# Performance work log

Measured on AMD Instinct MI355X. Metric: run time of the kernel, lower is better.

The kernel has to match this reference:

```python
import jax, jax.numpy as jnp
import numpy as np

N = 20000
E = 320000
F_IN = 256
HID = 32
HEADS = 8
EDGE_DIM = HID // 4  # 8
NEG_SLOPE = 0.2


def _gat_conv(x, src, dst, e_emb, W, att_s, att_d, W_e, att_e, bias, H, C):
    """PyG-style GATConv with edge_dim, add_self_loops=True (fill_value='mean'), concat heads."""
    n = x.shape[0]
    loop = jnp.arange(n, dtype=src.dtype)
    # self-loop edge_attr = scatter-mean of edge_attr by dst (0 for isolated nodes)
    deg = jax.ops.segment_sum(jnp.ones_like(dst, dtype=x.dtype), dst, num_segments=n)
    e_mean = jax.ops.segment_sum(e_emb, dst, num_segments=n) / jnp.maximum(deg, 1.0)[:, None]
    src_a = jnp.concatenate([src, loop])
    dst_a = jnp.concatenate([dst, loop])
    e_all = jnp.concatenate([e_emb, e_mean], axis=0)  # [E+N, edge_dim]

    h = (x @ W).reshape(n, H, C)                      # [N,H,C]
    a_src = jnp.einsum('nhc,hc->nh', h, att_s)        # [N,H]
    a_dst = jnp.einsum('nhc,hc->nh', h, att_d)
    he = (e_all @ W_e).reshape(-1, H, C)              # [E+N,H,C]
    a_edge = jnp.einsum('ehc,hc->eh', he, att_e)      # [E+N,H]

    alpha = jax.nn.leaky_relu(a_src[src_a] + a_dst[dst_a] + a_edge, NEG_SLOPE)
    # segment softmax over destination nodes
    amax = jax.ops.segment_max(alpha, dst_a, num_segments=n)
    alpha = jnp.exp(alpha - amax[dst_a])
    denom = jax.ops.segment_sum(alpha, dst_a, num_segments=n)
    alpha = alpha / (denom[dst_a] + 1e-16)

    msg = h[src_a] * alpha[:, :, None]                # [E+N,H,C]
    out = jax.ops.segment_sum(msg, dst_a, num_segments=n)  # [N,H,C]
    return out.reshape(n, H * C) + bias


def setup_inputs() -> dict:
    key = jax.random.key(0)
    ks = jax.random.split(key, 16)

    def glorot(k, shape):
        fan_in, fan_out = shape[0], shape[-1]
        s = np.sqrt(6.0 / (fan_in + fan_out))
        return jax.random.uniform(k, shape, jnp.float32, -s, s)

    x = jax.random.normal(ks[0], (N, F_IN), jnp.float32)
    edge_index = jax.random.randint(ks[1], (2, E), 0, N, jnp.int32)
    edge_attr = jax.random.uniform(ks[2], (E, 2), jnp.float32)

    # spatial_embed: Linear(2 -> EDGE_DIM)
    Wse = glorot(ks[3], (2, EDGE_DIM))
    bse = jnp.zeros((EDGE_DIM,), jnp.float32)
    # conv1: in=F_IN, heads=HEADS, out=HID, edge_dim=EDGE_DIM
    W1 = glorot(ks[4], (F_IN, HEADS * HID))
    as1 = glorot(ks[5], (HEADS, HID))
    ad1 = glorot(ks[6], (HEADS, HID))
    We1 = glorot(ks[7], (EDGE_DIM, HEADS * HID))
    ae1 = glorot(ks[8], (HEADS, HID))
    b1 = jnp.zeros((HEADS * HID,), jnp.float32)
    # conv2: in=HEADS*HID, heads=1, out=HID
    W2 = glorot(ks[9], (HEADS * HID, HID))
    as2 = glorot(ks[10], (1, HID))
    ad2 = glorot(ks[11], (1, HID))
    We2 = glorot(ks[12], (EDGE_DIM, HID))
    ae2 = glorot(ks[13], (1, HID))
    b2 = jnp.zeros((HID,), jnp.float32)

    return {"x": x, "edge_index": edge_index, "edge_attr": edge_attr,
            "Wse": Wse, "bse": bse,
            "W1": W1, "as1": as1, "ad1": ad1, "We1": We1, "ae1": ae1, "b1": b1,
            "W2": W2, "as2": as2, "ad2": ad2, "We2": We2, "ae2": ae2, "b2": b2}


def reference(x, edge_index, edge_attr, Wse, bse,
              W1, as1, ad1, We1, ae1, b1,
              W2, as2, ad2, We2, ae2, b2):
    src, dst = edge_index[0], edge_index[1]
    e = jax.nn.relu(edge_attr @ Wse + bse)            # [E, EDGE_DIM]
    h = _gat_conv(x, src, dst, e, W1, as1, ad1, We1, ae1, b1, HEADS, HID)
    h = jax.nn.relu(h)                                # dropout inactive (eval)
    out = _gat_conv(h, src, dst, e, W2, as2, ad2, We2, ae2, b2, 1, HID)
    return out
```

## Files before the change

### kernel.cpp

```cpp
#include <hip/hip_runtime.h>
#include <hip/hip_bf16.h>
#include <hip/hip_fp16.h>
#include <float.h>


typedef short v8s __attribute__((ext_vector_type(8)));
typedef float v4f __attribute__((ext_vector_type(4)));

__device__ __forceinline__ ushort f2bf(float f) {
  unsigned u = __float_as_uint(f);
  u = (u + 0x7FFF + ((u >> 16) & 1)) >> 16;
  return (ushort)u;
}
__device__ __forceinline__ float bf2f(ushort h) {
  return __uint_as_float(((unsigned)h) << 16);
}
__device__ __forceinline__ unsigned pk2bf(float lo, float hi) {
  return (unsigned)f2bf(lo) | ((unsigned)f2bf(hi) << 16);
}
__device__ __forceinline__ unsigned pk2h(float lo, float hi) {
  return (unsigned)__half_as_ushort(__float2half(lo)) |
         ((unsigned)__half_as_ushort(__float2half(hi)) << 16);
}

__global__ __launch_bounds__(256) void k_pre(const int* __restrict__ dst,
                                             const float* __restrict__ W1,
                                             const float* __restrict__ We1,
                                             const float* __restrict__ ae1,
                                             const float* __restrict__ We2,
                                             const float* __restrict__ ae2,
                                             const float* __restrict__ W2,
                                             int* __restrict__ deg,
                                             ushort* __restrict__ Bt,
                                             float* __restrict__ M1,
                                             float* __restrict__ m2,
                                             float* __restrict__ W2B,
                                             int E, int DB) {
  int b = blockIdx.x;
  if (b < DB) {
    int e = b * 256 + threadIdx.x;
    if (e < E) atomicAdd(&deg[dst[e]], 1);
    return;
  }
  if (b == DB + 64) {
    int t = threadIdx.x;
    for (int i = t; i < 8192; i += 256) {
      int k = i >> 5, cc = i & 31;
      W2B[(size_t)(k >> 2) * 128 + cc * 4 + (k & 3)] = W2[(size_t)k * 32 + cc];
    }
    if (t < 64) {
      int k = t >> 3, h = t & 7;
      float s = 0.f;
      for (int c = 0; c < 32; c++) s += We1[k * 256 + h * 32 + c] * ae1[h * 32 + c];
      M1[k * 8 + h] = s;
    } else if (t < 72) {
      int k = t - 64;
      float s = 0.f;
      for (int c = 0; c < 32; c++) s += We2[k * 32 + c] * ae2[c];
      m2[k] = s;
    }
    return;
  }
  int b2 = b - DB;
  __shared__ float tile[32][33];
  int bx = b2 & 7, by = b2 >> 3;
  int tx = threadIdx.x & 31, ty = threadIdx.x >> 5;
  for (int r = ty; r < 32; r += 8)
    tile[r][tx] = W1[(size_t)(by * 32 + r) * 256 + bx * 32 + tx];
  __syncthreads();
  for (int r = ty; r < 32; r += 8)
    Bt[(size_t)(bx * 32 + r) * 256 + by * 32 + tx] = f2bf(tile[tx][r]);
}

__global__ __launch_bounds__(1024) void k_scan(const int* __restrict__ deg,
                                               int* __restrict__ row_ptr,
                                               int* __restrict__ cursor, int N) {
  __shared__ int part[1024];
  int tid = threadIdx.x;
  int chunk = (N + 1023) / 1024;
  int lo = tid * chunk;
  if (lo > N) lo = N;
  int hi = lo + chunk;
  if (hi > N) hi = N;
  int s = 0;
  for (int i = lo; i < hi; i++) { s += deg[i]; cursor[i] = 0; }
  part[tid] = s;
  __syncthreads();
  for (int off = 1; off < 1024; off <<= 1) {
    int v = 0;
    if (tid >= off) v = part[tid - off];
    __syncthreads();
    part[tid] += v;
    __syncthreads();
  }
  int base = part[tid] - s;
  for (int i = lo; i < hi; i++) { row_ptr[i] = base; base += deg[i]; }
  if (tid == 1023) row_ptr[N] = part[1023];
}

__global__ __launch_bounds__(256) void k_mega1(
    const float* __restrict__ A, const ushort* __restrict__ Bt,
    const float* __restrict__ as1, const float* __restrict__ ad1,
    ushort* __restrict__ h1b, float* __restrict__ asv, float* __restrict__ adv, int M,
    const int* __restrict__ src, const int* __restrict__ dst,
    const float* __restrict__ ea, const float* __restrict__ Wse,
    const float* __restrict__ bse, const float* __restrict__ M1,
    const float* __restrict__ m2, const int* __restrict__ row_ptr,
    int* __restrict__ cursor, char* __restrict__ rec, int E, int GB) {
  __shared__ __align__(16) char smem[27648];
  int t = threadIdx.x;
  if (blockIdx.x >= GB) {
    float* sW  = (float*)smem;
    float* sbv = sW + 16;
    float* sM  = sbv + 8;
    float* sm2 = sM + 64;
    if (t < 16) sW[t] = Wse[t];
    if (t < 8) sbv[t] = bse[t];
    if (t < 64) sM[t] = M1[t];
    if (t >= 64 && t < 72) sm2[t - 64] = m2[t - 64];
    __syncthreads();
    int i = (blockIdx.x - GB) * 256 + t;
    if (i >= E) return;
    float2 av = ((const float2*)ea)[i];
    float e8[8];
#pragma unroll
    for (int k = 0; k < 8; k++)
      e8[k] = fmaxf(av.x * sW[k] + av.y * sW[8 + k] + sbv[k], 0.f);
    float o[8];
#pragma unroll
    for (int h = 0; h < 8; h++) {
      float s = 0.f;
#pragma unroll
      for (int k = 0; k < 8; k++) s += e8[k] * sM[k * 8 + h];
      o[h] = s;
    }
    float s2 = 0.f;
#pragma unroll
    for (int k = 0; k < 8; k++) s2 += e8[k] * sm2[k];
    int d = dst[i];
    int pos = row_ptr[d] + atomicAdd(&cursor[d], 1);
    uint4 w0, w1;
    w0.x = (unsigned)src[i];
    w0.y = pk2h(o[0], o[1]);
    w0.z = pk2h(o[2], o[3]);
    w0.w = pk2h(o[4], o[5]);
    w1.x = pk2h(o[6], o[7]);
    w1.y = __float_as_uint(s2);
    w1.z = 0; w1.w = 0;
    *(uint4*)(rec + (size_t)pos * 32)      = w0;
    *(uint4*)(rec + (size_t)pos * 32 + 16) = w1;
    return;
  }
  ushort* sA = (ushort*)smem;
  ushort* sB = (ushort*)(smem + 5120);
  float* sas = (float*)(smem + 25600);
  float* sad = (float*)(smem + 26624);
  int wave = t >> 6, lane = t & 63;
  int m0 = blockIdx.x * 64;
  int c = lane & 15, kg = lane >> 4;
  sas[t] = as1[t];
  sad[t] = ad1[t];
  v4f acc[4][4];
#pragma unroll
  for (int a = 0; a < 4; a++)
#pragma unroll
    for (int b = 0; b < 4; b++) acc[a][b] = (v4f)(0.f);
  int arow = t >> 2;
  int akoff = (t & 3) * 8;
  bool aval = (m0 + arow) < M;
  const float* aptr = A + (size_t)(m0 + arow) * 256 + akoff;
  const ushort* bptr = Bt + (size_t)t * 256;
  for (int k0 = 0; k0 < 256; k0 += 32) {
    float4 v0 = make_float4(0.f, 0.f, 0.f, 0.f), v1 = v0;
    if (aval) { v0 = *(const float4*)(aptr + k0); v1 = *(const float4*)(aptr + k0 + 4); }
    unsigned* dst32 = (unsigned*)&sA[arow * 40 + akoff];
    dst32[0] = pk2bf(v0.x, v0.y);
    dst32[1] = pk2bf(v0.z, v0.w);
    dst32[2] = pk2bf(v1.x, v1.y);
    dst32[3] = pk2bf(v1.z, v1.w);
    *(v8s*)&sB[t * 40 + 0]  = *(const v8s*)(bptr + k0 + 0);
    *(v8s*)&sB[t * 40 + 8]  = *(const v8s*)(bptr + k0 + 8);
    *(v8s*)&sB[t * 40 + 16] = *(const v8s*)(bptr + k0 + 16);
    *(v8s*)&sB[t * 40 + 24] = *(const v8s*)(bptr + k0 + 24);
    __syncthreads();
    v8s af[4], bfr[4];
#pragma unroll
    for (int mt = 0; mt < 4; mt++) af[mt] = *(v8s*)&sA[(mt * 16 + c) * 40 + kg * 8];
#pragma unroll
    for (int nt = 0; nt < 4; nt++) bfr[nt] = *(v8s*)&sB[(wave * 64 + nt * 16 + c) * 40 + kg * 8];
#pragma unroll
    for (int mt = 0; mt < 4; mt++)
#pragma unroll
      for (int nt = 0; nt < 4; nt++)
        acc[mt][nt] = __builtin_amdgcn_mfma_f32_16x16x32_bf16(af[mt], bfr[nt], acc[mt][nt], 0, 0, 0);
    __syncthreads();
  }
  int colbase = wave * 64;
#pragma unroll
  for (int mt = 0; mt < 4; mt++) {
#pragma unroll
    for (int i = 0; i < 4; i++) {
      int m = m0 + mt * 16 + kg * 4 + i;
      if (m < M) {
#pragma unroll
        for (int nt = 0; nt < 4; nt++)
          h1b[(size_t)m * 256 + colbase + nt * 16 + c] = f2bf(acc[mt][nt][i]);
      }
      float s1a = acc[mt][0][i] * sas[colbase + c]      + acc[mt][1][i] * sas[colbase + 16 + c];
      float s2a = acc[mt][0][i] * sad[colbase + c]      + acc[mt][1][i] * sad[colbase + 16 + c];
      float s1b = acc[mt][2][i] * sas[colbase + 32 + c] + acc[mt][3][i] * sas[colbase + 48 + c];
      float s2b = acc[mt][2][i] * sad[colbase + 32 + c] + acc[mt][3][i] * sad[colbase + 48 + c];
#pragma unroll
      for (int o = 1; o < 16; o <<= 1) {
        s1a += __shfl_xor(s1a, o);
        s2a += __shfl_xor(s2a, o);
        s1b += __shfl_xor(s1b, o);
        s2b += __shfl_xor(s2b, o);
      }
      if (c == 0 && m < M) {
        asv[(size_t)m * 8 + 2 * wave]     = s1a;
        adv[(size_t)m * 8 + 2 * wave]     = s2a;
        asv[(size_t)m * 8 + 2 * wave + 1] = s1b;
        adv[(size_t)m * 8 + 2 * wave + 1] = s2b;
      }
    }
  }
}

__global__ __launch_bounds__(64) void k_conv1(
    const int* __restrict__ row_ptr, const char* __restrict__ rec,
    const float* __restrict__ asv, const float* __restrict__ adv,
    const ushort* __restrict__ h1b, const float* __restrict__ b1,
    const float* __restrict__ W2B, const float* __restrict__ as2,
    const float* __restrict__ ad2, float* __restrict__ g2,
    float* __restrict__ asv2, float* __restrict__ adv2, int N) {
  int n = blockIdx.x;
  int lane = threadIdx.x;
  int h = lane >> 3;
  int sub = lane & 7;
  int hh = lane & 7;
  __shared__ float sw[64 * 8];
  __shared__ int ssrc[64];
  __shared__ float sm[8], sl[8], sadv[8], smean[8];
  __shared__ float sh2[256];
  int begin = row_ptr[n], end = row_ptr[n + 1];
  int degr = end - begin;
  if (lane < 8) { sm[lane] = -FLT_MAX; sl[lane] = 0.f; sadv[lane] = adv[(size_t)n * 8 + lane]; }
  float aedsum = 0.f;
  float4 acc = make_float4(0.f, 0.f, 0.f, 0.f);
  for (int cs = begin; cs < end; cs += 64) {
    int c = min(64, end - cs);
    __syncthreads();
    if (lane < c) ssrc[lane] = *(const int*)(rec + (size_t)(cs + lane) * 32);
    __syncthreads();
    for (int idx = lane; idx < c * 8; idx += 64) {
      int el = idx >> 3;
      float ae = __half2float(*(const __half*)(rec + (size_t)(cs + el) * 32 + 4 + hh * 2));
      aedsum += ae;
      float a = asv[(size_t)ssrc[el] * 8 + hh] + sadv[hh] + ae;
      a = a > 0.f ? a : 0.2f * a;
      sw[idx] = a;
    }
    __syncthreads();
    float mloc = -FLT_MAX;
    for (int el = sub; el < c; el += 8) mloc = fmaxf(mloc, sw[el * 8 + h]);
#pragma unroll
    for (int o = 1; o < 8; o <<= 1) mloc = fmaxf(mloc, __shfl_xor(mloc, o));
    float mold = sm[h];
    float mnew = fmaxf(mold, mloc);
    float scale = __expf(mold - mnew);
    float lloc = 0.f;
    for (int el = sub; el < c; el += 8) {
      float w = __expf(sw[el * 8 + h] - mnew);
      sw[el * 8 + h] = w;
      lloc += w;
    }
#pragma unroll
    for (int o = 1; o < 8; o <<= 1) lloc += __shfl_xor(lloc, o);
    __syncthreads();
    if (sub == 0) { sm[h] = mnew; sl[h] = sl[h] * scale + lloc; }
    acc.x *= scale; acc.y *= scale; acc.z *= scale; acc.w *= scale;
#pragma unroll 2
    for (int el = 0; el < c; el++) {
      float w = sw[el * 8 + h];
      ushort4 hv = *(const ushort4*)(h1b + (size_t)ssrc[el] * 256 + lane * 4);
      acc.x += w * bf2f(hv.x);
      acc.y += w * bf2f(hv.y);
      acc.z += w * bf2f(hv.z);
      acc.w += w * bf2f(hv.w);
    }
  }
  aedsum += __shfl_xor(aedsum, 8);
  aedsum += __shfl_xor(aedsum, 16);
  aedsum += __shfl_xor(aedsum, 32);
  float invd = 1.f / (float)(degr > 1 ? degr : 1);
  if (lane < 8) smean[lane] = aedsum * invd;
  __syncthreads();
  float a_self = asv[(size_t)n * 8 + h] + sadv[h] + smean[h];
  a_self = a_self > 0.f ? a_self : 0.2f * a_self;
  float mold = sm[h];
  float mnew = fmaxf(mold, a_self);
  float scale = __expf(mold - mnew);
  float w_self = __expf(a_self - mnew);
  float l_fin = sl[h] * scale + w_self;
  ushort4 hs = *(const ushort4*)(h1b + (size_t)n * 256 + lane * 4);
  acc.x = acc.x * scale + w_self * bf2f(hs.x);
  acc.y = acc.y * scale + w_self * bf2f(hs.y);
  acc.z = acc.z * scale + w_self * bf2f(hs.z);
  acc.w = acc.w * scale + w_self * bf2f(hs.w);
  float inv = 1.f / (l_fin + 1e-16f);
  float4 bv = *(const float4*)(b1 + lane * 4);
  float4 h2v;
  h2v.x = fmaxf(acc.x * inv + bv.x, 0.f);
  h2v.y = fmaxf(acc.y * inv + bv.y, 0.f);
  h2v.z = fmaxf(acc.z * inv + bv.z, 0.f);
  h2v.w = fmaxf(acc.w * inv + bv.w, 0.f);
  *(float4*)&sh2[lane * 4] = h2v;
  __syncthreads();
  int half = lane >> 5, cc = lane & 31;
  const float* wp = W2B + (size_t)half * 32 * 128 + cc * 4;
  const float* hp2 = sh2 + half * 128;
  float part = 0.f;
#pragma unroll 8
  for (int g = 0; g < 32; g++) {
    float4 wv = *(const float4*)(wp + g * 128);
    float4 hv = *(const float4*)(hp2 + g * 4);
    part += wv.x * hv.x + wv.y * hv.y + wv.z * hv.z + wv.w * hv.w;
  }
  part += __shfl_xor(part, 32);
  float s1 = part * as2[cc];
  float s2 = part * ad2[cc];
#pragma unroll
  for (int o = 1; o < 32; o <<= 1) {
    s1 += __shfl_xor(s1, o);
    s2 += __shfl_xor(s2, o);
  }
  if (lane < 32) g2[(size_t)n * 32 + cc] = part;
  if (lane == 0) { asv2[n] = s1; adv2[n] = s2; }
}

__global__ __launch_bounds__(64) void k_conv2(
    const int* __restrict__ row_ptr, const char* __restrict__ rec,
    const float* __restrict__ asv2, const float* __restrict__ adv2,
    const float* __restrict__ g2, const float* __restrict__ b2,
    float* __restrict__ out, int N) {
  int n = blockIdx.x;
  int lane = threadIdx.x;
  int sub = lane >> 3, q = lane & 7;
  __shared__ float sw[64];
  __shared__ int ssrc[64];
  int begin = row_ptr[n], end = row_ptr[n + 1];
  int degr = end - begin;
  float advn = adv2[n];
  float m = -FLT_MAX, l = 0.f, aedsum = 0.f;
  float4 acc = make_float4(0.f, 0.f, 0.f, 0.f);
  for (int cs = begin; cs < end; cs += 64) {
    int c = min(64, end - cs);
    __syncthreads();
    float a = -FLT_MAX;
    if (lane < c) {
      const char* rp = rec + (size_t)(cs + lane) * 32;
      int s = *(const int*)rp;
      ssrc[lane] = s;
      float ae = *(const float*)(rp + 20);
      aedsum += ae;
      a = asv2[s] + advn + ae;
      a = a > 0.f ? a : 0.2f * a;
    }
    float cm = a;
#pragma unroll
    for (int o = 1; o < 64; o <<= 1) cm = fmaxf(cm, __shfl_xor(cm, o));
    float nm = fmaxf(m, cm);
    float sc = __expf(m - nm);
    float w = (lane < c) ? __expf(a - nm) : 0.f;
    float cl = w;
#pragma unroll
    for (int o = 1; o < 64; o <<= 1) cl += __shfl_xor(cl, o);
    l = l * sc + cl;
    m = nm;
    sw[lane] = w;
    __syncthreads();
    acc.x *= sc; acc.y *= sc; acc.z *= sc; acc.w *= sc;
    for (int el = sub; el < c; el += 8) {
      float w2 = sw[el];
      const float4 gv = *(const float4*)(g2 + (size_t)ssrc[el] * 32 + q * 4);
      acc.x += w2 * gv.x; acc.y += w2 * gv.y; acc.z += w2 * gv.z; acc.w += w2 * gv.w;
    }
  }
#pragma unroll
  for (int o = 1; o < 64; o <<= 1) aedsum += __shfl_xor(aedsum, o);
  float invd = 1.f / (float)(degr > 1 ? degr : 1);
  float a_self = asv2[n] + advn + aedsum * invd;
  a_self = a_self > 0.f ? a_self : 0.2f * a_self;
  float nm = fmaxf(m, a_self);
  float sc = __expf(m - nm);
  float w_self = __expf(a_self - nm);
  l = l * sc + w_self;
  acc.x *= sc; acc.y *= sc; acc.z *= sc; acc.w *= sc;
  if (sub == 0) {
    const float4 gv = *(const float4*)(g2 + (size_t)n * 32 + q * 4);
    acc.x += w_self * gv.x; acc.y += w_self * gv.y;
    acc.z += w_self * gv.z; acc.w += w_self * gv.w;
  }
#pragma unroll
  for (int o = 8; o < 64; o <<= 1) {
    acc.x += __shfl_xor(acc.x, o);
    acc.y += __shfl_xor(acc.y, o);
    acc.z += __shfl_xor(acc.z, o);
    acc.w += __shfl_xor(acc.w, o);
  }
  if (lane < 8) {
    float inv = 1.f / (l + 1e-16f);
    float4 bv = *(const float4*)(b2 + lane * 4);
    float4 o4;
    o4.x = acc.x * inv + bv.x;
    o4.y = acc.y * inv + bv.y;
    o4.z = acc.z * inv + bv.z;
    o4.w = acc.w * inv + bv.w;
    *(float4*)(out + (size_t)n * 32 + lane * 4) = o4;
  }
}

extern "C" void kernel_launch(void* const* d_in, const int* in_sizes, int n_in,
                              void* d_out, int out_size, void* d_ws, size_t ws_size,
                              hipStream_t stream) {
  (void)n_in; (void)out_size; (void)ws_size;
  const float* x   = (const float*)d_in[0];
  const int*   ei  = (const int*)d_in[1];
  const float* ea  = (const float*)d_in[2];
  const float* Wse = (const float*)d_in[3];
  const float* bse = (const float*)d_in[4];
  const float* W1  = (const float*)d_in[5];
  const float* as1 = (const float*)d_in[6];
  const float* ad1 = (const float*)d_in[7];
  const float* We1 = (const float*)d_in[8];
  const float* ae1 = (const float*)d_in[9];
  const float* b1  = (const float*)d_in[10];
  const float* W2  = (const float*)d_in[11];
  const float* as2 = (const float*)d_in[12];
  const float* ad2 = (const float*)d_in[13];
  const float* We2 = (const float*)d_in[14];
  const float* ae2 = (const float*)d_in[15];
  const float* b2  = (const float*)d_in[16];
  const int N = in_sizes[0] / 256;
  const int E = in_sizes[1] / 2;
  const int* src = ei;
  const int* dst = ei + E;

  char* base = (char*)d_ws;
  size_t off = 0;
  auto alloc = [&](size_t bytes) -> char* {
    off = (off + 255) & ~(size_t)255;
    char* p = base + off;
    off += bytes;
    return p;
  };
  int*   deg      = (int*)alloc((size_t)N * 4);
  int*   cursor   = (int*)alloc((size_t)N * 4);
  int* row_ptr    = (int*)alloc((size_t)(N + 1) * 4);
  char* rec       = alloc((size_t)E * 32);
  ushort* W1T     = (ushort*)alloc((size_t)256 * 256 * 2);
  float* W2B      = (float*)alloc((size_t)256 * 32 * 4);
  ushort* h1b     = (ushort*)alloc((size_t)N * 256 * 2);
  float* asv1     = (float*)alloc((size_t)N * 8 * 4);
  float* adv1     = (float*)alloc((size_t)N * 8 * 4);
  float* g2       = (float*)alloc((size_t)N * 32 * 4);
  float* asv2     = (float*)alloc((size_t)N * 4);
  float* adv2     = (float*)alloc((size_t)N * 4);
  float* M1       = (float*)alloc(64 * 4);
  float* m2       = (float*)alloc(8 * 4);

  const int DB = (E + 255) / 256;
  const int GB = (N + 63) / 64;
  hipMemsetAsync(deg, 0, (size_t)N * 4, stream);
  k_pre<<<DB + 65, 256, 0, stream>>>(dst, W1, We1, ae1, We2, ae2, W2,
                                     deg, W1T, M1, m2, W2B, E, DB);
  k_scan<<<1, 1024, 0, stream>>>(deg, row_ptr, cursor, N);
  k_mega1<<<GB + DB, 256, 0, stream>>>(x, W1T, as1, ad1, h1b, asv1, adv1, N,
                                       src, dst, ea, Wse, bse, M1, m2, row_ptr,
                                       cursor, rec, E, GB);
  k_conv1<<<N, 64, 0, stream>>>(row_ptr, rec, asv1, adv1, h1b, b1,
                                W2B, as2, ad2, g2, asv2, adv2, N);
  k_conv2<<<N, 64, 0, stream>>>(row_ptr, rec, asv2, adv2, g2, b2, (float*)d_out, N);
}
```

Baseline: 227.8 us.

## Pack four destination nodes per block in GAT conv kernels and batch gathers

Both aggregation kernels now run four nodes per 256-thread block, one wavefront each, instead of one 64-thread block per node. Chunk loops iterate to the block's maximum chunk count so __syncthreads stays uniform, and invalid or exhausted waves are masked. The conv1 gather loop is unrolled by eight to issue independent h1 row loads together, and conv2's gather gets unroll 2. This is meant to cut launch and scheduling overhead from very small blocks and raise memory-level parallelism. The cost is block-level syncs coupling waves, so a high-degree node stalls the other three waves in its block.

After: 245.0 us. +7.5%, slower.

```diff
diff --git a/kernel.cpp b/kernel.cpp
--- a/kernel.cpp
+++ b/kernel.cpp
@@ -227,63 +227,91 @@
   }
 }
 
-__global__ __launch_bounds__(64) void k_conv1(
+__global__ __launch_bounds__(256) void k_conv1(
     const int* __restrict__ row_ptr, const char* __restrict__ rec,
     const float* __restrict__ asv, const float* __restrict__ adv,
     const ushort* __restrict__ h1b, const float* __restrict__ b1,
     const float* __restrict__ W2B, const float* __restrict__ as2,
     const float* __restrict__ ad2, float* __restrict__ g2,
     float* __restrict__ asv2, float* __restrict__ adv2, int N) {
-  int n = blockIdx.x;
-  int lane = threadIdx.x;
+  int wid = threadIdx.x >> 6;
+  int lane = threadIdx.x & 63;
+  int n = blockIdx.x * 4 + wid;
+  bool valid = n < N;
   int h = lane >> 3;
   int sub = lane & 7;
   int hh = lane & 7;
-  __shared__ float sw[64 * 8];
-  __shared__ int ssrc[64];
-  __shared__ float sm[8], sl[8], sadv[8], smean[8];
-  __shared__ float sh2[256];
-  int begin = row_ptr[n], end = row_ptr[n + 1];
+  __shared__ float sw[4][64 * 8];
+  __shared__ int ssrc[4][64];
+  __shared__ float sm[4][8], sl[4][8], sadv[4][8], smean[4][8];
+  __shared__ float sh2[4][256];
+  __shared__ int snch[4];
+  int begin = 0, end = 0;
+  if (valid) { begin = row_ptr[n]; end = row_ptr[n + 1]; }
   int degr = end - begin;
-  if (lane < 8) { sm[lane] = -FLT_MAX; sl[lane] = 0.f; sadv[lane] = adv[(size_t)n * 8 + lane]; }
+  if (lane == 0) snch[wid] = (degr + 63) >> 6;
+  if (lane < 8) {
+    sm[wid][lane] = -FLT_MAX;
+    sl[wid][lane] = 0.f;
+    sadv[wid][lane] = valid ? adv[(size_t)n * 8 + lane] : 0.f;
+  }
+  __syncthreads();
+  int maxc = max(max(snch[0], snch[1]), max(snch[2], snch[3]));
   float aedsum = 0.f;
   float4 acc = make_float4(0.f, 0.f, 0.f, 0.f);
-  for (int cs = begin; cs < end; cs += 64) {
+  for (int ch = 0; ch < maxc; ch++) {
+    int cs = begin + ch * 64;
     int c = min(64, end - cs);
     __syncthreads();
-    if (lane < c) ssrc[lane] = *(const int*)(rec + (size_t)(cs + lane) * 32);
+    if (lane < c) ssrc[wid][lane] = *(const int*)(rec + (size_t)(cs + lane) * 32);
     __syncthreads();
     for (int idx = lane; idx < c * 8; idx += 64) {
       int el = idx >> 3;
       float ae = __half2float(*(const __half*)(rec + (size_t)(cs + el) * 32 + 4 + hh * 2));
       aedsum += ae;
-      float a = asv[(size_t)ssrc[el] * 8 + hh] + sadv[hh] + ae;
+      float a = asv[(size_t)ssrc[wid][el] * 8 + hh] + sadv[wid][hh] + ae;
       a = a > 0.f ? a : 0.2f * a;
-      sw[idx] = a;
+      sw[wid][idx] = a;
     }
     __syncthreads();
     float mloc = -FLT_MAX;
-    for (int el = sub; el < c; el += 8) mloc = fmaxf(mloc, sw[el * 8 + h]);
+    for (int el = sub; el < c; el += 8) mloc = fmaxf(mloc, sw[wid][el * 8 + h]);
 #pragma unroll
     for (int o = 1; o < 8; o <<= 1) mloc = fmaxf(mloc, __shfl_xor(mloc, o));
-    float mold = sm[h];
+    float mold = sm[wid][h];
     float mnew = fmaxf(mold, mloc);
     float scale = __expf(mold - mnew);
     float lloc = 0.f;
     for (int el = sub; el < c; el += 8) {
-      float w = __expf(sw[el * 8 + h] - mnew);
-      sw[el * 8 + h] = w;
+      float w = __expf(sw[wid][el * 8 + h] - mnew);
+      sw[wid][el * 8 + h] = w;
       lloc += w;
     }
 #pragma unroll
     for (int o = 1; o < 8; o <<= 1) lloc += __shfl_xor(lloc, o);
     __syncthreads();
-    if (sub == 0) { sm[h] = mnew; sl[h] = sl[h] * scale + lloc; }
+    if (sub == 0 && c > 0) { sm[wid][h] = mnew; sl[wid][h] = sl[wid][h] * scale + lloc; }
     acc.x *= scale; acc.y *= scale; acc.z *= scale; acc.w *= scale;
-#pragma unroll 2
-    for (int el = 0; el < c; el++) {
-      float w = sw[el * 8 + h];
-      ushort4 hv = *(const ushort4*)(h1b + (size_t)ssrc[el] * 256 + lane * 4);
+    int el = 0;
+    for (; el + 8 <= c; el += 8) {
+      float w[8];
+      ushort4 hv[8];
+#pragma unroll
+      for (int j = 0; j < 8; j++) w[j] = sw[wid][(el + j) * 8 + h];
+#pragma unroll
+      for (int j = 0; j < 8; j++)
+        hv[j] = *(const ushort4*)(h1b + (size_t)ssrc[wid][el + j] * 256 + lane * 4);
+#pragma unroll
+      for (int j = 0; j < 8; j++) {
+        acc.x += w[j] * bf2f(hv[j].x);
+        acc.y += w[j] * bf2f(hv[j].y);
+        acc.z += w[j] * bf2f(hv[j].z);
+        acc.w += w[j] * bf2f(hv[j].w);
+      }
+    }
+    for (; el < c; el++) {
+      float w = sw[wid][el * 8 + h];
+      ushort4 hv = *(const ushort4*)(h1b + (size_t)ssrc[wid][el] * 256 + lane * 4);
       acc.x += w * bf2f(hv.x);
       acc.y += w * bf2f(hv.y);
       acc.z += w * bf2f(hv.z);
@@ -294,74 +322,86 @@
   aedsum += __shfl_xor(aedsum, 16);
   aedsum += __shfl_xor(aedsum, 32);
   float invd = 1.f / (float)(degr > 1 ? degr : 1);
-  if (lane < 8) smean[lane] = aedsum * invd;
+  if (lane < 8) smean[wid][lane] = aedsum * invd;
   __syncthreads();
-  float a_self = asv[(size_t)n * 8 + h] + sadv[h] + smean[h];
-  a_self = a_self > 0.f ? a_self : 0.2f * a_self;
-  float mold = sm[h];
-  float mnew = fmaxf(mold, a_self);
-  float scale = __expf(mold - mnew);
-  float w_self = __expf(a_self - mnew);
-  float l_fin = sl[h] * scale + w_self;
-  ushort4 hs = *(const ushort4*)(h1b + (size_t)n * 256 + lane * 4);
-  acc.x = acc.x * scale + w_self * bf2f(hs.x);
-  acc.y = acc.y * scale + w_self * bf2f(hs.y);
-  acc.z = acc.z * scale + w_self * bf2f(hs.z);
-  acc.w = acc.w * scale + w_self * bf2f(hs.w);
-  float inv = 1.f / (l_fin + 1e-16f);
-  float4 bv = *(const float4*)(b1 + lane * 4);
-  float4 h2v;
-  h2v.x = fmaxf(acc.x * inv + bv.x, 0.f);
-  h2v.y = fmaxf(acc.y * inv + bv.y, 0.f);
-  h2v.z = fmaxf(acc.z * inv + bv.z, 0.f);
-  h2v.w = fmaxf(acc.w * inv + bv.w, 0.f);
-  *(float4*)&sh2[lane * 4] = h2v;
+  float4 h2v = make_float4(0.f, 0.f, 0.f, 0.f);
+  if (valid) {
+    float a_self = asv[(size_t)n * 8 + h] + sadv[wid][h] + smean[wid][h];
+    a_self = a_self > 0.f ? a_self : 0.2f * a_self;
+    float mold = sm[wid][h];
+    float mnew = fmaxf(mold, a_self);
+    float scale = __expf(mold - mnew);
+    float w_self = __expf(a_self - mnew);
+    float l_fin = sl[wid][h] * scale + w_self;
+    ushort4 hs = *(const ushort4*)(h1b + (size_t)n * 256 + lane * 4);
+    acc.x = acc.x * scale + w_self * bf2f(hs.x);
+    acc.y = acc.y * scale + w_self * bf2f(hs.y);
+    acc.z = acc.z * scale + w_self * bf2f(hs.z);
+    acc.w = acc.w * scale + w_self * bf2f(hs.w);
+    float inv = 1.f / (l_fin + 1e-16f);
+    float4 bv = *(const float4*)(b1 + lane * 4);
+    h2v.x = fmaxf(acc.x * inv + bv.x, 0.f);
+    h2v.y = fmaxf(acc.y * inv + bv.y, 0.f);
+    h2v.z = fmaxf(acc.z * inv + bv.z, 0.f);
+    h2v.w = fmaxf(acc.w * inv + bv.w, 0.f);
+  }
+  *(float4*)&sh2[wid][lane * 4] = h2v;
   __syncthreads();
-  int half = lane >> 5, cc = lane & 31;
-  const float* wp = W2B + (size_t)half * 32 * 128 + cc * 4;
-  const float* hp2 = sh2 + half * 128;
-  float part = 0.f;
+  if (valid) {
+    int half = lane >> 5, cc = lane & 31;
+    const float* wp = W2B + (size_t)half * 32 * 128 + cc * 4;
+    const float* hp2 = &sh2[wid][half * 128];
+    float part = 0.f;
 #pragma unroll 8
-  for (int g = 0; g < 32; g++) {
-    float4 wv = *(const float4*)(wp + g * 128);
-    float4 hv = *(const float4*)(hp2 + g * 4);
-    part += wv.x * hv.x + wv.y * hv.y + wv.z * hv.z + wv.w * hv.w;
-  }
-  part += __shfl_xor(part, 32);
-  float s1 = part * as2[cc];
-  float s2 = part * ad2[cc];
-#pragma unroll
-  for (int o = 1; o < 32; o <<= 1) {
-    s1 += __shfl_xor(s1, o);
-    s2 += __shfl_xor(s2, o);
-  }
-  if (lane < 32) g2[(size_t)n * 32 + cc] = part;
-  if (lane == 0) { asv2[n] = s1; adv2[n] = s2; }
-}
-
-__global__ __launch_bounds__(64) void k_conv2(
+    for (int g = 0; g < 32; g++) {
+      float4 wv = *(const float4*)(wp + g * 128);
+      float4 hv = *(const float4*)(hp2 + g * 4);
+      part += wv.x * hv.x + wv.y * hv.y + wv.z * hv.z + wv.w * hv.w;
+    }
+    part += __shfl_xor(part, 32);
+    float s1 = part * as2[cc];
+    float s2 = part * ad2[cc];
+#pragma unroll
+    for (int o = 1; o < 32; o <<= 1) {
+      s1 += __shfl_xor(s1, o);
+      s2 += __shfl_xor(s2, o);
+    }
+    if (lane < 32) g2[(size_t)n * 32 + cc] = part;
+    if (lane == 0) { asv2[n] = s1; adv2[n] = s2; }
+  }
+}
+
+__global__ __launch_bounds__(256) void k_conv2(
     const int* __restrict__ row_ptr, const char* __restrict__ rec,
     const float* __restrict__ asv2, const float* __restrict__ adv2,
     const float* __restrict__ g2, const float* __restrict__ b2,
     float* __restrict__ out, int N) {
-  int n = blockIdx.x;
-  int lane = threadIdx.x;
+  int wid = threadIdx.x >> 6;
+  int lane = threadIdx.x & 63;
+  int n = blockIdx.x * 4 + wid;
+  bool valid = n < N;
   int sub = lane >> 3, q = lane & 7;
-  __shared__ float sw[64];
-  __shared__ int ssrc[64];
-  int begin = row_ptr[n], end = row_ptr[n + 1];
+  __shared__ float sw[4][64];
+  __shared__ int ssrc[4][64];
+  __shared__ int snch[4];
+  int begin = 0, end = 0;
+  if (valid) { begin = row_ptr[n]; end = row_ptr[n + 1]; }
   int degr = end - begin;
-  float advn = adv2[n];
+  if (lane == 0) snch[wid] = (degr + 63) >> 6;
+  __syncthreads();
+  int maxc = max(max(snch[0], snch[1]), max(snch[2], snch[3]));
+  float advn = valid ? adv2[n] : 0.f;
   float m = -FLT_MAX, l = 0.f, aedsum = 0.f;
   float4 acc = make_float4(0.f, 0.f, 0.f, 0.f);
-  for (int cs = begin; cs < end; cs += 64) {
+  for (int ch = 0; ch < maxc; ch++) {
+    int cs = begin + ch * 64;
     int c = min(64, end - cs);
     __syncthreads();
     float a = -FLT_MAX;
     if (lane < c) {
       const char* rp = rec + (size_t)(cs + lane) * 32;
       int s = *(const int*)rp;
-      ssrc[lane] = s;
+      ssrc[wid][lane] = s;
       float ae = *(const float*)(rp + 20);
       aedsum += ae;
       a = asv2[s] + advn + ae;
@@ -378,46 +418,49 @@
     for (int o = 1; o < 64; o <<= 1) cl += __shfl_xor(cl, o);
     l = l * sc + cl;
     m = nm;
-    sw[lane] = w;
+    sw[wid][lane] = w;
     __syncthreads();
     acc.x *= sc; acc.y *= sc; acc.z *= sc; acc.w *= sc;
+#pragma unroll 2
     for (int el = sub; el < c; el += 8) {
-      float w2 = sw[el];
-      const float4 gv = *(const float4*)(g2 + (size_t)ssrc[el] * 32 + q * 4);
+      float w2 = sw[wid][el];
+      const float4 gv = *(const float4*)(g2 + (size_t)ssrc[wid][el] * 32 + q * 4);
       acc.x += w2 * gv.x; acc.y += w2 * gv.y; acc.z += w2 * gv.z; acc.w += w2 * gv.w;
     }
   }
 #pragma unroll
   for (int o = 1; o < 64; o <<= 1) aedsum += __shfl_xor(aedsum, o);
-  float invd = 1.f / (float)(degr > 1 ? degr : 1);
-  float a_self = asv2[n] + advn + aedsum * invd;
-  a_self = a_self > 0.f ? a_self : 0.2f * a_self;
-  float nm = fmaxf(m, a_self);
-  float sc = __expf(m - nm);
-  float w_self = __expf(a_self - nm);
-  l = l * sc + w_self;
-  acc.x *= sc; acc.y *= sc; acc.z *= sc; acc.w *= sc;
-  if (sub == 0) {
-    const float4 gv = *(const float4*)(g2 + (size_t)n * 32 + q * 4);
-    acc.x += w_self * gv.x; acc.y += w_self * gv.y;
-    acc.z += w_self * gv.z; acc.w += w_self * gv.w;
-  }
-#pragma unroll
-  for (int o = 8; o < 64; o <<= 1) {
-    acc.x += __shfl_xor(acc.x, o);
-    acc.y += __shfl_xor(acc.y, o);
-    acc.z += __shfl_xor(acc.z, o);
-    acc.w += __shfl_xor(acc.w, o);
-  }
-  if (lane < 8) {
-    float inv = 1.f / (l + 1e-16f);
-    float4 bv = *(const float4*)(b2 + lane * 4);
-    float4 o4;
-    o4.x = acc.x * inv + bv.x;
-    o4.y = acc.y * inv + bv.y;
-    o4.z = acc.z * inv + bv.z;
-    o4.w = acc.w * inv + bv.w;
-    *(float4*)(out + (size_t)n * 32 + lane * 4) = o4;
+  if (valid) {
+    float invd = 1.f / (float)(degr > 1 ? degr : 1);
+    float a_self = asv2[n] + advn + aedsum * invd;
+    a_self = a_self > 0.f ? a_self : 0.2f * a_self;
+    float nm = fmaxf(m, a_self);
+    float sc = __expf(m - nm);
+    float w_self = __expf(a_self - nm);
+    l = l * sc + w_self;
+    acc.x *= sc; acc.y *= sc; acc.z *= sc; acc.w *= sc;
+    if (sub == 0) {
+      const float4 gv = *(const float4*)(g2 + (size_t)n * 32 + q * 4);
+      acc.x += w_self * gv.x; acc.y += w_self * gv.y;
+      acc.z += w_self * gv.z; acc.w += w_self * gv.w;
+    }
+#pragma unroll
+    for (int o = 8; o < 64; o <<= 1) {
+      acc.x += __shfl_xor(acc.x, o);
+      acc.y += __shfl_xor(acc.y, o);
+      acc.z += __shfl_xor(acc.z, o);
+      acc.w += __shfl_xor(acc.w, o);
+    }
+    if (lane < 8) {
+      float inv = 1.f / (l + 1e-16f);
+      float4 bv = *(const float4*)(b2 + lane * 4);
+      float4 o4;
+      o4.x = acc.x * inv + bv.x;
+      o4.y = acc.y * inv + bv.y;
+      o4.z = acc.z * inv + bv.z;
+      o4.w = acc.w * inv + bv.w;
+      *(float4*)(out + (size_t)n * 32 + lane * 4) = o4;
+    }
   }
 }
 
@@ -479,7 +522,8 @@
   k_mega1<<<GB + DB, 256, 0, stream>>>(x, W1T, as1, ad1, h1b, asv1, adv1, N,
                                        src, dst, ea, Wse, bse, M1, m2, row_ptr,
                                        cursor, rec, E, GB);
-  k_conv1<<<N, 64, 0, stream>>>(row_ptr, rec, asv1, adv1, h1b, b1,
-                                W2B, as2, ad2, g2, asv2, adv2, N);
-  k_conv2<<<N, 64, 0, stream>>>(row_ptr, rec, asv2, adv2, g2, b2, (float*)d_out, N);
-}
+  k_conv1<<<(N + 3) / 4, 256, 0, stream>>>(row_ptr, rec, asv1, adv1, h1b, b1,
+                                           W2B, as2, ad2, g2, asv2, adv2, N);
+  k_conv2<<<(N + 3) / 4, 256, 0, stream>>>(row_ptr, rec, asv2, adv2, g2, b2,
+                                           (float*)d_out, N);
+}
```
